# Optimization experiments

Measured on AMD Instinct MI355X. Metric: run time of the kernel, lower is better.

The kernel has to match this reference:

```python
import jax, jax.numpy as jnp
import numpy as np

N = 12288
F_IN = 128
F_OUT = 128


def setup_inputs() -> dict:
    key = jax.random.key(0)
    k1, k2, k3, k4, k5, k6, k7 = jax.random.split(key, 7)
    stdv = 1.0 / np.sqrt(F_OUT)
    return {
        "feats": jax.random.normal(k1, (N, F_IN), dtype=jnp.float32),
        "node_adj": jax.random.normal(k2, (N, N), dtype=jnp.float32),
        "edge_adj": jax.random.normal(k3, (N, N), dtype=jnp.float32),
        # params: msg_type='concat' -> node_weight is [2*in, out]
        "node_weight": jax.random.uniform(k4, (2 * F_IN, F_OUT), dtype=jnp.float32, minval=-stdv, maxval=stdv),
        "node_bias": jax.random.uniform(k5, (F_OUT,), dtype=jnp.float32, minval=-stdv, maxval=stdv),
        "edge_weight": jax.random.uniform(k6, (F_IN, F_OUT), dtype=jnp.float32, minval=-stdv, maxval=stdv),
        "edge_bias": jax.random.uniform(k7, (F_OUT,), dtype=jnp.float32, minval=-stdv, maxval=stdv),
    }


def reference(feats, node_adj, edge_adj, node_weight, node_bias, edge_weight, edge_bias):
    # msg_type == 'concat': two masked spmms over signed adjacency, concat along features
    pos = (node_adj > 0).astype(feats.dtype)  # [N, N]
    neg = (node_adj < 0).astype(feats.dtype)  # [N, N]
    node_support = jnp.concatenate([pos @ feats, neg @ feats], axis=1)  # [N, 2*F_IN]
    node_output = node_support @ node_weight + node_bias  # [N, F_OUT]
    edge_support = edge_adj @ feats  # [N, F_IN]
    edge_output = edge_support @ edge_weight + edge_bias  # [N, F_OUT]
    return jax.nn.relu(node_output) + edge_output
```

## Files before the change

kernel.cpp:

```cpp
#include <hip/hip_runtime.h>
#include <stdint.h>

#define N_ROWS 12288
#define GSZ (128 * 12288)
#define NPART_OFF (9437184 / 4)
#define EPART_OFF ((9437184 + 6291456) / 4)

typedef __attribute__((ext_vector_type(8))) short bf16x8;
typedef __attribute__((ext_vector_type(4))) float f32x4;

__device__ __forceinline__ uint32_t f2bf(float x) {
  union { float f; uint32_t u; } c; c.f = x;
  return (c.u + 0x7FFFu + ((c.u >> 16) & 1u)) >> 16;
}
__device__ __forceinline__ uint32_t pk_bf(float a, float b) {
  return f2bf(a) | (f2bf(b) << 16);
}
__device__ __forceinline__ uint32_t pk_pos(float a, float b) {
  return (a > 0.f ? 0x3F80u : 0u) | (b > 0.f ? 0x3F800000u : 0u);
}
__device__ __forceinline__ uint32_t pk_neg(float a, float b) {
  return (a < 0.f ? 0x3F80u : 0u) | (b < 0.f ? 0x3F800000u : 0u);
}

__global__ __launch_bounds__(256) void gw_kernel(
    const float* __restrict__ feats, const float* __restrict__ node_w,
    const float* __restrict__ edge_w, uint16_t* __restrict__ gt) {
  __shared__ float lf[16 * 128];
  const int t = threadIdx.x;
  const int kb = blockIdx.x * 16;
  {
    const float4* src = (const float4*)(feats + (size_t)kb * 128);
    float4* dst = (float4*)lf;
    dst[t] = src[t];
    dst[t + 256] = src[t + 256];
  }
  __syncthreads();
  const int n = t & 127;
  const int rh = t >> 7;
  const float* wb[3] = {node_w, node_w + 128 * 128, edge_w};
#pragma unroll
  for (int j = 0; j < 3; ++j) {
    const float* W = wb[j] + n;
    float acc[8];
#pragma unroll
    for (int q = 0; q < 8; ++q) acc[q] = 0.f;
    for (int i = 0; i < 128; i += 4) {
      const float w0 = W[(i + 0) * 128];
      const float w1 = W[(i + 1) * 128];
      const float w2 = W[(i + 2) * 128];
      const float w3 = W[(i + 3) * 128];
#pragma unroll
      for (int q = 0; q < 8; ++q) {
        const float4 f = *(const float4*)&lf[(rh * 8 + q) * 128 + i];
        acc[q] = fmaf(f.w, w3, fmaf(f.z, w2, fmaf(f.y, w1, fmaf(f.x, w0, acc[q]))));
      }
    }
    uint4 o;
    o.x = pk_bf(acc[0], acc[1]);
    o.y = pk_bf(acc[2], acc[3]);
    o.z = pk_bf(acc[4], acc[5]);
    o.w = pk_bf(acc[6], acc[7]);
    *(uint4*)(gt + (size_t)j * GSZ + (size_t)n * N_ROWS + kb + rh * 8) = o;
  }
}

__global__ __launch_bounds__(256, 4) void fgc_main(
    const float* __restrict__ node_adj, const float* __restrict__ edge_adj,
    const uint16_t* __restrict__ gt, float* __restrict__ node_part,
    float* __restrict__ edge_part) {
  __shared__ __align__(128) char smem[24576];
  const int t = threadIdx.x;
  const int l = t & 63;
  const int w = t >> 6;
  const int bid = blockIdx.x;
  const int slice = bid & 7;
  const int row0 = (bid >> 3) * 64;
  const size_t k0 = (size_t)slice * 1536;

  const int r = t >> 2, o = t & 3;
  const float* np_ = node_adj + (size_t)(row0 + r) * N_ROWS + k0 + o * 8;
  const float* ep_ = edge_adj + (size_t)(row0 + r) * N_ROWS + k0 + o * 8;
  const int wOff = r * 64 + ((o ^ ((r >> 2) & 3)) * 16);

  const int r15 = l & 15;
  const int gq = l >> 4;
  const int abase = r15 * 64 + ((gq ^ ((r15 >> 2) & 3)) * 16);

  const uint16_t* gB = gt + (size_t)(w * 32 + r15) * N_ROWS + k0 + gq * 8;

  f32x4 accn[4][2], acce[4][2];
#pragma unroll
  for (int a = 0; a < 4; ++a)
#pragma unroll
    for (int b = 0; b < 2; ++b) {
      accn[a][b] = {0.f, 0.f, 0.f, 0.f};
      acce[a][b] = {0.f, 0.f, 0.f, 0.f};
    }

  float4 rn0, rn1, re0, re1;
  rn0 = *(const float4*)(np_);
  rn1 = *(const float4*)(np_ + 4);
  re0 = *(const float4*)(ep_);
  re1 = *(const float4*)(ep_ + 4);

  for (int kt = 0; kt < 48; ++kt) {
    char* wb2 = smem + (kt & 1) * 12288;
    {
      uint4 P, Q, E;
      P.x = pk_pos(rn0.x, rn0.y); P.y = pk_pos(rn0.z, rn0.w);
      P.z = pk_pos(rn1.x, rn1.y); P.w = pk_pos(rn1.z, rn1.w);
      Q.x = pk_neg(rn0.x, rn0.y); Q.y = pk_neg(rn0.z, rn0.w);
      Q.z = pk_neg(rn1.x, rn1.y); Q.w = pk_neg(rn1.z, rn1.w);
      E.x = pk_bf(re0.x, re0.y);  E.y = pk_bf(re0.z, re0.w);
      E.z = pk_bf(re1.x, re1.y);  E.w = pk_bf(re1.z, re1.w);
      *(uint4*)(wb2 + wOff) = P;
      *(uint4*)(wb2 + 4096 + wOff) = Q;
      *(uint4*)(wb2 + 8192 + wOff) = E;
    }
    __syncthreads();
    if (kt < 47) {
      const size_t ko = (size_t)(kt + 1) * 32;
      rn0 = *(const float4*)(np_ + ko);
      rn1 = *(const float4*)(np_ + ko + 4);
      re0 = *(const float4*)(ep_ + ko);
      re1 = *(const float4*)(ep_ + ko + 4);
    }
    const char* rb = smem + (kt & 1) * 12288;
    bf16x8 ap[4], an[4], ae[4];
#pragma unroll
    for (int mf = 0; mf < 4; ++mf) {
      ap[mf] = *(const bf16x8*)(rb + abase + mf * 1024);
      an[mf] = *(const bf16x8*)(rb + 4096 + abase + mf * 1024);
      ae[mf] = *(const bf16x8*)(rb + 8192 + abase + mf * 1024);
    }
    const uint16_t* gk = gB + kt * 32;
#pragma unroll
    for (int nf = 0; nf < 2; ++nf) {
      const uint16_t* gp = gk + (size_t)nf * 16 * N_ROWS;
      const bf16x8 b1 = *(const bf16x8*)(gp);
      const bf16x8 b2 = *(const bf16x8*)(gp + GSZ);
      const bf16x8 b3 = *(const bf16x8*)(gp + 2 * GSZ);
#pragma unroll
      for (int mf = 0; mf < 4; ++mf)
        accn[mf][nf] = __builtin_amdgcn_mfma_f32_16x16x32_bf16(ap[mf], b1, accn[mf][nf], 0, 0, 0);
#pragma unroll
      for (int mf = 0; mf < 4; ++mf)
        accn[mf][nf] = __builtin_amdgcn_mfma_f32_16x16x32_bf16(an[mf], b2, accn[mf][nf], 0, 0, 0);
#pragma unroll
      for (int mf = 0; mf < 4; ++mf)
        acce[mf][nf] = __builtin_amdgcn_mfma_f32_16x16x32_bf16(ae[mf], b3, acce[mf][nf], 0, 0, 0);
    }
  }

#pragma unroll
  for (int nf = 0; nf < 2; ++nf) {
    const int col = w * 32 + nf * 16 + r15;
#pragma unroll
    for (int mf = 0; mf < 4; ++mf) {
      const f32x4 nv = accn[mf][nf];
      const f32x4 ev = acce[mf][nf];
#pragma unroll
      for (int q = 0; q < 4; ++q) {
        const size_t idx = (size_t)(row0 + mf * 16 + gq * 4 + q) * 128 + col;
        unsafeAtomicAdd(&node_part[idx], nv[q]);
        unsafeAtomicAdd(&edge_part[idx], ev[q]);
      }
    }
  }
}

__global__ __launch_bounds__(256) void fgc_final(
    const float* __restrict__ node_part, const float* __restrict__ edge_part,
    const float* __restrict__ node_bias, const float* __restrict__ edge_bias,
    float* __restrict__ out) {
  const int idx = blockIdx.x * 256 + threadIdx.x;
  const int col = (idx * 4) & 127;
  const float4 n = ((const float4*)node_part)[idx];
  const float4 e = ((const float4*)edge_part)[idx];
  const float4 nb = *(const float4*)(node_bias + col);
  const float4 eb = *(const float4*)(edge_bias + col);
  float4 o;
  o.x = fmaxf(n.x + nb.x, 0.f) + e.x + eb.x;
  o.y = fmaxf(n.y + nb.y, 0.f) + e.y + eb.y;
  o.z = fmaxf(n.z + nb.z, 0.f) + e.z + eb.z;
  o.w = fmaxf(n.w + nb.w, 0.f) + e.w + eb.w;
  ((float4*)out)[idx] = o;
}

extern "C" void kernel_launch(void* const* d_in, const int* in_sizes, int n_in,
                              void* d_out, int out_size, void* d_ws, size_t ws_size,
                              hipStream_t stream) {
  const float* feats = (const float*)d_in[0];
  const float* node_adj = (const float*)d_in[1];
  const float* edge_adj = (const float*)d_in[2];
  const float* node_w = (const float*)d_in[3];
  const float* node_b = (const float*)d_in[4];
  const float* edge_w = (const float*)d_in[5];
  const float* edge_b = (const float*)d_in[6];
  uint16_t* gt = (uint16_t*)d_ws;
  float* node_part = (float*)d_ws + NPART_OFF;
  float* edge_part = (float*)d_ws + EPART_OFF;

  gw_kernel<<<768, 256, 0, stream>>>(feats, node_w, edge_w, gt);
  hipMemsetAsync((char*)d_ws + 9437184, 0, 2 * 6291456, stream);
  fgc_main<<<1536, 256, 0, stream>>>(node_adj, edge_adj, gt,
                                     node_part, edge_part);
  fgc_final<<<1536, 256, 0, stream>>>(node_part, edge_part, node_b, edge_b,
                                      (float*)d_out);
}
```

Baseline: 418.2 us.

## Double block to 512 threads, split node/edge loaders, unroll k-loop by two

The main kernel now runs 512 threads per block. The first half loads and packs node_adj and the second half edge_adj, and each wave owns 16 output columns instead of 32. The k-loop is manually unrolled by two with even/odd shared buffers, B fragments are prefetched into registers a stage ahead, and adjacency prefetch is issued two stages ahead. Raw s_barrier plus sched_barrier calls replace __syncthreads. The aim is to keep more loads in flight to hide HBM latency on the adjacency stream, at the cost of more waves and more barrier synchronisation per block.

```diff
diff --git a/kernel.cpp b/kernel.cpp
--- a/kernel.cpp
+++ b/kernel.cpp
@@ -22,6 +22,8 @@
 __device__ __forceinline__ uint32_t pk_neg(float a, float b) {
   return (a < 0.f ? 0x3F80u : 0u) | (b < 0.f ? 0x3F800000u : 0u);
 }
+
+#define MFMA __builtin_amdgcn_mfma_f32_16x16x32_bf16
 
 __global__ __launch_bounds__(256) void gw_kernel(
     const float* __restrict__ feats, const float* __restrict__ node_w,
@@ -56,16 +58,16 @@
         acc[q] = fmaf(f.w, w3, fmaf(f.z, w2, fmaf(f.y, w1, fmaf(f.x, w0, acc[q]))));
       }
     }
-    uint4 o;
-    o.x = pk_bf(acc[0], acc[1]);
-    o.y = pk_bf(acc[2], acc[3]);
-    o.z = pk_bf(acc[4], acc[5]);
-    o.w = pk_bf(acc[6], acc[7]);
-    *(uint4*)(gt + (size_t)j * GSZ + (size_t)n * N_ROWS + kb + rh * 8) = o;
-  }
-}
-
-__global__ __launch_bounds__(256, 4) void fgc_main(
+    uint4 ov;
+    ov.x = pk_bf(acc[0], acc[1]);
+    ov.y = pk_bf(acc[2], acc[3]);
+    ov.z = pk_bf(acc[4], acc[5]);
+    ov.w = pk_bf(acc[6], acc[7]);
+    *(uint4*)(gt + (size_t)j * GSZ + (size_t)n * N_ROWS + kb + rh * 8) = ov;
+  }
+}
+
+__global__ __launch_bounds__(512, 4) void fgc_main(
     const float* __restrict__ node_adj, const float* __restrict__ edge_adj,
     const uint16_t* __restrict__ gt, float* __restrict__ node_part,
     float* __restrict__ edge_part) {
@@ -76,96 +78,143 @@
   const int bid = blockIdx.x;
   const int slice = bid & 7;
   const int row0 = (bid >> 3) * 64;
-  const size_t k0 = (size_t)slice * 1536;
-
-  const int r = t >> 2, o = t & 3;
-  const float* np_ = node_adj + (size_t)(row0 + r) * N_ROWS + k0 + o * 8;
-  const float* ep_ = edge_adj + (size_t)(row0 + r) * N_ROWS + k0 + o * 8;
-  const int wOff = r * 64 + ((o ^ ((r >> 2) & 3)) * 16);
+  const int k0 = slice * 1536;
+
+  const int ts = t & 255;
+  const int r = ts >> 2, o = ts & 3;
+  const bool isNode = (t < 256);
+  const float* src = (isNode ? node_adj : edge_adj) +
+                     (size_t)(row0 + r) * N_ROWS + k0 + o * 8;
+  const int wOff = r * 64 + ((o ^ ((r >> 1) & 3)) * 16);
 
   const int r15 = l & 15;
   const int gq = l >> 4;
-  const int abase = r15 * 64 + ((gq ^ ((r15 >> 2) & 3)) * 16);
-
-  const uint16_t* gB = gt + (size_t)(w * 32 + r15) * N_ROWS + k0 + gq * 8;
-
-  f32x4 accn[4][2], acce[4][2];
-#pragma unroll
-  for (int a = 0; a < 4; ++a)
-#pragma unroll
-    for (int b = 0; b < 2; ++b) {
-      accn[a][b] = {0.f, 0.f, 0.f, 0.f};
-      acce[a][b] = {0.f, 0.f, 0.f, 0.f};
-    }
-
-  float4 rn0, rn1, re0, re1;
-  rn0 = *(const float4*)(np_);
-  rn1 = *(const float4*)(np_ + 4);
-  re0 = *(const float4*)(ep_);
-  re1 = *(const float4*)(ep_ + 4);
-
-  for (int kt = 0; kt < 48; ++kt) {
-    char* wb2 = smem + (kt & 1) * 12288;
+  const int abase = r15 * 64 + ((gq ^ ((r15 >> 1) & 3)) * 16);
+
+  const uint16_t* gB = gt + (size_t)(w * 16 + r15) * N_ROWS + k0 + gq * 8;
+
+  f32x4 accn[4], acce[4];
+#pragma unroll
+  for (int a = 0; a < 4; ++a) {
+    accn[a] = {0.f, 0.f, 0.f, 0.f};
+    acce[a] = {0.f, 0.f, 0.f, 0.f};
+  }
+
+  float4 x0, x1, y0, y1;
+  x0 = *(const float4*)(src);
+  x1 = *(const float4*)(src + 4);
+  y0 = *(const float4*)(src + 32);
+  y1 = *(const float4*)(src + 36);
+  bf16x8 bev1, bev2, bev3, bod1, bod2, bod3;
+  bev1 = *(const bf16x8*)(gB);
+  bev2 = *(const bf16x8*)(gB + GSZ);
+  bev3 = *(const bf16x8*)(gB + 2 * GSZ);
+
+#pragma unroll 1
+  for (int k2 = 0; k2 < 24; ++k2) {
+    const int kt = k2 * 2;
+    if (isNode) {
+      uint4 P, Q;
+      P.x = pk_pos(x0.x, x0.y); P.y = pk_pos(x0.z, x0.w);
+      P.z = pk_pos(x1.x, x1.y); P.w = pk_pos(x1.z, x1.w);
+      Q.x = pk_neg(x0.x, x0.y); Q.y = pk_neg(x0.z, x0.w);
+      Q.z = pk_neg(x1.x, x1.y); Q.w = pk_neg(x1.z, x1.w);
+      *(uint4*)(smem + wOff) = P;
+      *(uint4*)(smem + 4096 + wOff) = Q;
+    } else {
+      uint4 E;
+      E.x = pk_bf(x0.x, x0.y); E.y = pk_bf(x0.z, x0.w);
+      E.z = pk_bf(x1.x, x1.y); E.w = pk_bf(x1.z, x1.w);
+      *(uint4*)(smem + 8192 + wOff) = E;
+    }
+    asm volatile("s_waitcnt lgkmcnt(0)" ::: "memory");
+    __builtin_amdgcn_s_barrier();
     {
-      uint4 P, Q, E;
-      P.x = pk_pos(rn0.x, rn0.y); P.y = pk_pos(rn0.z, rn0.w);
-      P.z = pk_pos(rn1.x, rn1.y); P.w = pk_pos(rn1.z, rn1.w);
-      Q.x = pk_neg(rn0.x, rn0.y); Q.y = pk_neg(rn0.z, rn0.w);
-      Q.z = pk_neg(rn1.x, rn1.y); Q.w = pk_neg(rn1.z, rn1.w);
-      E.x = pk_bf(re0.x, re0.y);  E.y = pk_bf(re0.z, re0.w);
-      E.z = pk_bf(re1.x, re1.y);  E.w = pk_bf(re1.z, re1.w);
-      *(uint4*)(wb2 + wOff) = P;
-      *(uint4*)(wb2 + 4096 + wOff) = Q;
-      *(uint4*)(wb2 + 8192 + wOff) = E;
-    }
-    __syncthreads();
-    if (kt < 47) {
-      const size_t ko = (size_t)(kt + 1) * 32;
-      rn0 = *(const float4*)(np_ + ko);
-      rn1 = *(const float4*)(np_ + ko + 4);
-      re0 = *(const float4*)(ep_ + ko);
-      re1 = *(const float4*)(ep_ + ko + 4);
-    }
-    const char* rb = smem + (kt & 1) * 12288;
-    bf16x8 ap[4], an[4], ae[4];
-#pragma unroll
-    for (int mf = 0; mf < 4; ++mf) {
-      ap[mf] = *(const bf16x8*)(rb + abase + mf * 1024);
-      an[mf] = *(const bf16x8*)(rb + 4096 + abase + mf * 1024);
-      ae[mf] = *(const bf16x8*)(rb + 8192 + abase + mf * 1024);
-    }
-    const uint16_t* gk = gB + kt * 32;
-#pragma unroll
-    for (int nf = 0; nf < 2; ++nf) {
-      const uint16_t* gp = gk + (size_t)nf * 16 * N_ROWS;
-      const bf16x8 b1 = *(const bf16x8*)(gp);
-      const bf16x8 b2 = *(const bf16x8*)(gp + GSZ);
-      const bf16x8 b3 = *(const bf16x8*)(gp + 2 * GSZ);
-#pragma unroll
-      for (int mf = 0; mf < 4; ++mf)
-        accn[mf][nf] = __builtin_amdgcn_mfma_f32_16x16x32_bf16(ap[mf], b1, accn[mf][nf], 0, 0, 0);
-#pragma unroll
-      for (int mf = 0; mf < 4; ++mf)
-        accn[mf][nf] = __builtin_amdgcn_mfma_f32_16x16x32_bf16(an[mf], b2, accn[mf][nf], 0, 0, 0);
-#pragma unroll
-      for (int mf = 0; mf < 4; ++mf)
-        acce[mf][nf] = __builtin_amdgcn_mfma_f32_16x16x32_bf16(ae[mf], b3, acce[mf][nf], 0, 0, 0);
-    }
-  }
-
-#pragma unroll
-  for (int nf = 0; nf < 2; ++nf) {
-    const int col = w * 32 + nf * 16 + r15;
-#pragma unroll
-    for (int mf = 0; mf < 4; ++mf) {
-      const f32x4 nv = accn[mf][nf];
-      const f32x4 ev = acce[mf][nf];
-#pragma unroll
-      for (int q = 0; q < 4; ++q) {
-        const size_t idx = (size_t)(row0 + mf * 16 + gq * 4 + q) * 128 + col;
-        unsafeAtomicAdd(&node_part[idx], nv[q]);
-        unsafeAtomicAdd(&edge_part[idx], ev[q]);
-      }
+      const uint16_t* gk = gB + (kt + 1) * 32;
+      bod1 = *(const bf16x8*)(gk);
+      bod2 = *(const bf16x8*)(gk + GSZ);
+      bod3 = *(const bf16x8*)(gk + 2 * GSZ);
+    }
+    __builtin_amdgcn_sched_barrier(0);
+    if (kt + 2 < 48) {
+      const float* s2 = src + (kt + 2) * 32;
+      x0 = *(const float4*)(s2);
+      x1 = *(const float4*)(s2 + 4);
+    }
+    __builtin_amdgcn_sched_barrier(0);
+    {
+      const char* rb = smem;
+      bf16x8 ap[4], an[4], ae[4];
+#pragma unroll
+      for (int mf = 0; mf < 4; ++mf) {
+        ap[mf] = *(const bf16x8*)(rb + abase + mf * 1024);
+        an[mf] = *(const bf16x8*)(rb + 4096 + abase + mf * 1024);
+        ae[mf] = *(const bf16x8*)(rb + 8192 + abase + mf * 1024);
+      }
+#pragma unroll
+      for (int mf = 0; mf < 4; ++mf) {
+        accn[mf] = MFMA(ap[mf], bev1, accn[mf], 0, 0, 0);
+        accn[mf] = MFMA(an[mf], bev2, accn[mf], 0, 0, 0);
+        acce[mf] = MFMA(ae[mf], bev3, acce[mf], 0, 0, 0);
+      }
+    }
+    if (isNode) {
+      uint4 P, Q;
+      P.x = pk_pos(y0.x, y0.y); P.y = pk_pos(y0.z, y0.w);
+      P.z = pk_pos(y1.x, y1.y); P.w = pk_pos(y1.z, y1.w);
+      Q.x = pk_neg(y0.x, y0.y); Q.y = pk_neg(y0.z, y0.w);
+      Q.z = pk_neg(y1.x, y1.y); Q.w = pk_neg(y1.z, y1.w);
+      *(uint4*)(smem + 12288 + wOff) = P;
+      *(uint4*)(smem + 12288 + 4096 + wOff) = Q;
+    } else {
+      uint4 E;
+      E.x = pk_bf(y0.x, y0.y); E.y = pk_bf(y0.z, y0.w);
+      E.z = pk_bf(y1.x, y1.y); E.w = pk_bf(y1.z, y1.w);
+      *(uint4*)(smem + 12288 + 8192 + wOff) = E;
+    }
+    asm volatile("s_waitcnt lgkmcnt(0)" ::: "memory");
+    __builtin_amdgcn_s_barrier();
+    if (kt + 2 < 48) {
+      const uint16_t* gk = gB + (kt + 2) * 32;
+      bev1 = *(const bf16x8*)(gk);
+      bev2 = *(const bf16x8*)(gk + GSZ);
+      bev3 = *(const bf16x8*)(gk + 2 * GSZ);
+    }
+    __builtin_amdgcn_sched_barrier(0);
+    if (kt + 3 < 48) {
+      const float* s3 = src + (kt + 3) * 32;
+      y0 = *(const float4*)(s3);
+      y1 = *(const float4*)(s3 + 4);
+    }
+    __builtin_amdgcn_sched_barrier(0);
+    {
+      const char* rb = smem + 12288;
+      bf16x8 ap[4], an[4], ae[4];
+#pragma unroll
+      for (int mf = 0; mf < 4; ++mf) {
+        ap[mf] = *(const bf16x8*)(rb + abase + mf * 1024);
+        an[mf] = *(const bf16x8*)(rb + 4096 + abase + mf * 1024);
+        ae[mf] = *(const bf16x8*)(rb + 8192 + abase + mf * 1024);
+      }
+#pragma unroll
+      for (int mf = 0; mf < 4; ++mf) {
+        accn[mf] = MFMA(ap[mf], bod1, accn[mf], 0, 0, 0);
+        accn[mf] = MFMA(an[mf], bod2, accn[mf], 0, 0, 0);
+        acce[mf] = MFMA(ae[mf], bod3, acce[mf], 0, 0, 0);
+      }
+    }
+  }
+
+  const int col = w * 16 + r15;
+#pragma unroll
+  for (int mf = 0; mf < 4; ++mf) {
+    const f32x4 nv = accn[mf];
+    const f32x4 ev = acce[mf];
+#pragma unroll
+    for (int q = 0; q < 4; ++q) {
+      const size_t idx = (size_t)(row0 + mf * 16 + gq * 4 + q) * 128 + col;
+      unsafeAtomicAdd(&node_part[idx], nv[q]);
+      unsafeAtomicAdd(&edge_part[idx], ev[q]);
     }
   }
 }
@@ -204,7 +253,7 @@
 
   gw_kernel<<<768, 256, 0, stream>>>(feats, node_w, edge_w, gt);
   hipMemsetAsync((char*)d_ws + 9437184, 0, 2 * 6291456, stream);
-  fgc_main<<<1536, 256, 0, stream>>>(node_adj, edge_adj, gt,
+  fgc_main<<<1536, 512, 0, stream>>>(node_adj, edge_adj, gt,
                                      node_part, edge_part);
   fgc_final<<<1536, 256, 0, stream>>>(node_part, edge_part, node_b, edge_b,
                                       (float*)d_out);
```

Result: slower. 453.2 us (+8.4%).
